# Kernel optimization log

Hardware: AMD Instinct MI355X
Metric: run time of the kernel (lower is better)

Reference implementation:

```python
import jax, jax.numpy as jnp
import numpy as np

B, H, OUT = 16384, 1024, 128
W_SCALE = 0.03  # ~1/sqrt(H) so attention logits / softmax stay well-conditioned


def setup_inputs() -> dict:
    key = jax.random.key(0)
    ks = jax.random.split(key, 12)
    return {
        "f1": jax.random.normal(ks[0], (B, H), jnp.float32),
        "f2": jax.random.normal(ks[1], (B, H), jnp.float32),
        "f3": jax.random.normal(ks[2], (B, H), jnp.float32),
        "f4": jax.random.normal(ks[3], (B, H), jnp.float32),
        "Wq": jax.random.normal(ks[4], (H, H), jnp.float32) * W_SCALE,
        "bq": jax.random.normal(ks[5], (H,), jnp.float32) * W_SCALE,
        "Wk": jax.random.normal(ks[6], (H, H), jnp.float32) * W_SCALE,
        "bk": jax.random.normal(ks[7], (H,), jnp.float32) * W_SCALE,
        "Wv": jax.random.normal(ks[8], (H, H), jnp.float32) * W_SCALE,
        "bv": jax.random.normal(ks[9], (H,), jnp.float32) * W_SCALE,
        "Wfc": jax.random.normal(ks[10], (H, OUT), jnp.float32) * W_SCALE,
        "bfc": jax.random.normal(ks[11], (OUT,), jnp.float32) * W_SCALE,
    }


def reference(f1, f2, f3, f4, Wq, bq, Wk, bk, Wv, bv, Wfc, bfc):
    # Stack the 4 backbone features: z [B, 4, H]
    z = jnp.stack([f1, f2, f3, f4], axis=1)
    q = z @ Wq + bq            # [B, 4, H]
    k = z @ Wk + bk            # [B, 4, H]
    v = z @ Wv + bv            # [B, 4, H]
    # Tiny 4x4 self-attention over the 4 model-feature tokens
    score = jax.nn.softmax(jnp.einsum('bth,bsh->bts', q, k), axis=-1)  # [B,4,4]
    att = jnp.einsum('bts,bsh->bth', score, v)                          # [B,4,H]
    x = jnp.sum(att, axis=1)                                            # [B,H]
    out = jax.nn.softmax(x @ Wfc + bfc, axis=-1)                        # [B,OUT]
    return (x, out)
```

## Files before the change

### kernel.cpp

```cpp
#include <hip/hip_runtime.h>
#include <hip/hip_bf16.h>
#include <stdint.h>

#define B_SZ 16384
#define H_SZ 1024
#define OUT_SZ 128

typedef __attribute__((ext_vector_type(4))) float f32x4;
typedef __attribute__((ext_vector_type(8))) _Float16 h16x8;
typedef unsigned short u16;
typedef unsigned int u32;

__device__ __forceinline__ u16 f2h(float f) {
  union { _Float16 h; u16 u; } v; v.h = (_Float16)f; return v.u;
}
__device__ __forceinline__ float h2f(u16 u) {
  union { u16 u; _Float16 h; } v; v.u = u; return (float)v.h;
}
__device__ __forceinline__ u32 pk2(float a, float b) {
  return (u32)f2h(a) | ((u32)f2h(b) << 16);
}

__device__ __forceinline__ void gl_lds16(const void* g, void* l) {
  __builtin_amdgcn_global_load_lds(
      (const __attribute__((address_space(1))) u32*)g,
      (__attribute__((address_space(3))) u32*)l, 16, 0, 0);
}

template<int MODE>
__global__ __launch_bounds__(256, 4) void gemm_nt(
    const u16* __restrict__ Aptr, const u16* __restrict__ Bptr,
    int N, int K,
    float* __restrict__ ep_f, u16* __restrict__ ep_b,
    const float* __restrict__ ep_v,
    const float* zf0, const float* zf1, const float* zf2, const float* zf3)
{
  constexpr int BM = 128, BN = 128, BK = 32;
  __shared__ __align__(16) u16 sA[2][BM * BK];
  __shared__ __align__(16) u16 sB[2][BN * BK];
  const int tid  = threadIdx.x;
  const int wave = tid >> 6;
  const int lane = tid & 63;
  const int qd   = lane >> 4;
  const int c16  = lane & 15;
  const int bm0  = blockIdx.x * BM;
  const int bn0  = blockIdx.y * BN;
  const int wm   = (wave >> 1) * 64;
  const int wn   = (wave & 1) * 64;
  const size_t FBS = (size_t)B_SZ * H_SZ;

  auto stage = [&](int buf, int k0) {
#pragma unroll
    for (int i = 0; i < 2; ++i) {
      int slot = tid + i * 256;
      int r = slot >> 2, pp = slot & 3;
      int cc = pp ^ ((r >> 1) & 3);
      {
        int gm = bm0 + r;
        const u16* gp;
        if (MODE == 1)
          gp = Aptr + (size_t)(gm & 3) * FBS + (size_t)(gm >> 2) * H_SZ + (k0 + cc * 8);
        else
          gp = Aptr + (size_t)gm * K + (k0 + cc * 8);
        gl_lds16(gp, &sA[buf][(size_t)(slot & ~63) * 8]);
      }
      {
        int gn = bn0 + r;
        const u16* gp = Bptr + (size_t)gn * K + (k0 + cc * 8);
        gl_lds16(gp, &sB[buf][(size_t)(slot & ~63) * 8]);
      }
    }
  };

  f32x4 acc[4][4];
#pragma unroll
  for (int i = 0; i < 4; ++i)
#pragma unroll
    for (int j = 0; j < 4; ++j)
      acc[i][j] = (f32x4){0.f, 0.f, 0.f, 0.f};

  stage(0, 0);
  __syncthreads();
  int cur = 0;
  for (int k0 = 0; k0 < K; k0 += BK) {
    if (k0 + BK < K) stage(cur ^ 1, k0 + BK);
    h16x8 af[4], bfr[4];
#pragma unroll
    for (int im = 0; im < 4; ++im) {
      int m = wm + im * 16 + c16;
      int slot = m * 4 + (qd ^ ((m >> 1) & 3));
      af[im] = *(const h16x8*)&sA[cur][slot * 8];
    }
#pragma unroll
    for (int in = 0; in < 4; ++in) {
      int n = wn + in * 16 + c16;
      int slot = n * 4 + (qd ^ ((n >> 1) & 3));
      bfr[in] = *(const h16x8*)&sB[cur][slot * 8];
    }
#pragma unroll
    for (int im = 0; im < 4; ++im)
#pragma unroll
      for (int in = 0; in < 4; ++in)
        acc[im][in] = __builtin_amdgcn_mfma_f32_16x16x32_f16(af[im], bfr[in], acc[im][in], 0, 0, 0);
    __syncthreads();
    cur ^= 1;
  }

  if constexpr (MODE == 0) {
#pragma unroll
    for (int im = 0; im < 4; ++im)
#pragma unroll
      for (int in = 0; in < 4; ++in) {
        int n = bn0 + wn + in * 16 + c16;
#pragma unroll
        for (int r = 0; r < 4; ++r) {
          int m = bm0 + wm + im * 16 + qd * 4 + r;
          ep_b[(size_t)m * N + n] = f2h(acc[im][in][r]);
        }
      }
  } else if constexpr (MODE == 1) {
    const float* zf[4] = {zf0, zf1, zf2, zf3};
    const int yg = (int)blockIdx.y * 2 + (wn >> 6);
#pragma unroll
    for (int im = 0; im < 4; ++im) {
      int mrow = bm0 + wm + im * 16 + qd * 4;
      size_t b = (size_t)(mrow >> 2);
      float p[4][4];
#pragma unroll
      for (int r = 0; r < 4; ++r)
#pragma unroll
        for (int s = 0; s < 4; ++s) p[r][s] = 0.f;
#pragma unroll
      for (int in = 0; in < 4; ++in) {
        int n = bn0 + wn + in * 16 + c16;
        float akv = ep_v[n];
        float rv[4];
#pragma unroll
        for (int r = 0; r < 4; ++r) rv[r] = acc[im][in][r] + akv;
#pragma unroll
        for (int s = 0; s < 4; ++s) {
          float zv = zf[s][b * H_SZ + n];
#pragma unroll
          for (int r = 0; r < 4; ++r) p[r][s] += rv[r] * zv;
        }
      }
#pragma unroll
      for (int r = 0; r < 4; ++r)
#pragma unroll
        for (int s = 0; s < 4; ++s) {
          float v = p[r][s];
          v += __shfl_xor(v, 1);
          v += __shfl_xor(v, 2);
          v += __shfl_xor(v, 4);
          v += __shfl_xor(v, 8);
          if (c16 == 0) ep_f[(b * 16 + (size_t)(r * 4 + s)) * 16 + yg] = v;
        }
    }
  } else if constexpr (MODE == 2) {
#pragma unroll
    for (int im = 0; im < 4; ++im)
#pragma unroll
      for (int in = 0; in < 4; ++in) {
        int n = bn0 + wn + in * 16 + c16;
        float bvv = 4.0f * ep_v[n];
#pragma unroll
        for (int r = 0; r < 4; ++r) {
          int m = bm0 + wm + im * 16 + qd * 4 + r;
          float v = acc[im][in][r] + bvv;
          ep_f[(size_t)m * H_SZ + n] = v;
          ep_b[(size_t)m * H_SZ + n] = f2h(v);
        }
      }
  } else {
#pragma unroll
    for (int im = 0; im < 4; ++im)
#pragma unroll
      for (int in = 0; in < 4; ++in) {
        int n = bn0 + wn + in * 16 + c16;
        float bc = ep_v[n];
#pragma unroll
        for (int r = 0; r < 4; ++r) {
          int m = bm0 + wm + im * 16 + qd * 4 + r;
          ep_f[(size_t)m * N + n] = acc[im][in][r] + bc;
        }
      }
  }
}

__global__ __launch_bounds__(256) void prep_weights(
    const float* __restrict__ Wq, const float* __restrict__ Wk,
    const float* __restrict__ Wv, const float* __restrict__ Wfc,
    const float* __restrict__ bq,
    u16* __restrict__ Wq16, u16* __restrict__ Wk16,
    u16* __restrict__ WvT, u16* __restrict__ WfcT,
    float* __restrict__ ak)
{
  __shared__ float t[32][33];
  int blk = blockIdx.x, tid = threadIdx.x;
  if (blk < 2048) {
    const float* src = (blk < 1024) ? Wq : Wk;
    u16* dst = (blk < 1024) ? Wq16 : Wk16;
    size_t i0 = (size_t)(blk & 1023) * 1024 + tid * 4;
    float4 v = *(const float4*)(src + i0);
    *(uint2*)(dst + i0) = make_uint2(pk2(v.x, v.y), pk2(v.z, v.w));
  } else if (blk < 3200) {
    int lx = tid & 31, ly = tid >> 5;
    if (blk < 3072) {
      int ti = blk - 2048;
      int tx = ti & 31, ty = ti >> 5;
#pragma unroll
      for (int k = 0; k < 4; ++k)
        t[ly + 8 * k][lx] = Wv[(size_t)(ty * 32 + ly + 8 * k) * 1024 + tx * 32 + lx];
      __syncthreads();
#pragma unroll
      for (int k = 0; k < 4; ++k)
        WvT[(size_t)(tx * 32 + ly + 8 * k) * 1024 + ty * 32 + lx] = f2h(t[lx][ly + 8 * k]);
    } else {
      int ti = blk - 3072;
      int tx = ti & 3, ty = ti >> 2;
#pragma unroll
      for (int k = 0; k < 4; ++k)
        t[ly + 8 * k][lx] = Wfc[(size_t)(ty * 32 + ly + 8 * k) * 128 + tx * 32 + lx];
      __syncthreads();
#pragma unroll
      for (int k = 0; k < 4; ++k)
        WfcT[(size_t)(tx * 32 + ly + 8 * k) * 1024 + ty * 32 + lx] = f2h(t[lx][ly + 8 * k]);
    }
  } else {
    int wave = tid >> 6, lane = tid & 63;
    int row = (blk - 3200) * 4 + wave;
    float s = 0.f;
    for (int i = lane; i < 1024; i += 64)
      s += Wk[(size_t)row * 1024 + i] * bq[i];
#pragma unroll
    for (int m = 1; m < 64; m <<= 1) s += __shfl_xor(s, m);
    if (lane == 0) ak[row] = s;
  }
}

__global__ __launch_bounds__(256) void convert4(
    const float* __restrict__ f1, const float* __restrict__ f2,
    const float* __restrict__ f3, const float* __restrict__ f4,
    u16* __restrict__ Zh)
{
  int a = blockIdx.x >> 13;
  const float* f = (a == 0) ? f1 : (a == 1) ? f2 : (a == 2) ? f3 : f4;
  size_t off = (size_t)(blockIdx.x & 8191) * 2048 + threadIdx.x * 8;
  float4 v0 = *(const float4*)(f + off);
  float4 v1 = *(const float4*)(f + off + 4);
  *(uint4*)(Zh + (size_t)a * B_SZ * H_SZ + off) =
      make_uint4(pk2(v0.x, v0.y), pk2(v0.z, v0.w), pk2(v1.x, v1.y), pk2(v1.z, v1.w));
}

__global__ __launch_bounds__(256) void softmax_g(
    const float* __restrict__ pl, const u16* __restrict__ Zh,
    u16* __restrict__ G)
{
  const size_t FBS = (size_t)B_SZ * H_SZ;
  int wave = threadIdx.x >> 6, lane = threadIdx.x & 63;
  size_t b = (size_t)blockIdx.x * 4 + wave;
  float4 pv = *(const float4*)(pl + b * 256 + (size_t)lane * 4);
  float part = pv.x + pv.y + pv.z + pv.w;
  part += __shfl_xor(part, 1);
  part += __shfl_xor(part, 2);
  float l[16];
#pragma unroll
  for (int i = 0; i < 16; ++i) l[i] = __shfl(part, i * 4);
  float w0 = 0, w1 = 0, w2 = 0, w3 = 0;
#pragma unroll
  for (int t = 0; t < 4; ++t) {
    float a0 = l[t * 4], a1 = l[t * 4 + 1], a2 = l[t * 4 + 2], a3 = l[t * 4 + 3];
    float mx = fmaxf(fmaxf(a0, a1), fmaxf(a2, a3));
    float e0 = __expf(a0 - mx), e1 = __expf(a1 - mx), e2 = __expf(a2 - mx), e3 = __expf(a3 - mx);
    float inv = 1.0f / (e0 + e1 + e2 + e3);
    w0 += e0 * inv; w1 += e1 * inv; w2 += e2 * inv; w3 += e3 * inv;
  }
#pragma unroll
  for (int ch = 0; ch < 2; ++ch) {
    size_t h0 = (size_t)lane * 8 + ch * 512;
    float g[8];
#pragma unroll
    for (int j = 0; j < 8; ++j) g[j] = 0.f;
#pragma unroll
    for (int s = 0; s < 4; ++s) {
      float ws = (s == 0) ? w0 : (s == 1) ? w1 : (s == 2) ? w2 : w3;
      uint4 zz = *(const uint4*)(Zh + (size_t)s * FBS + b * H_SZ + h0);
      u32 zs[4] = {zz.x, zz.y, zz.z, zz.w};
#pragma unroll
      for (int j = 0; j < 4; ++j) {
        g[2 * j]     += ws * h2f((u16)(zs[j] & 0xffffu));
        g[2 * j + 1] += ws * h2f((u16)(zs[j] >> 16));
      }
    }
    *(uint4*)(G + b * H_SZ + h0) =
        make_uint4(pk2(g[0], g[1]), pk2(g[2], g[3]), pk2(g[4], g[5]), pk2(g[6], g[7]));
  }
}

__global__ __launch_bounds__(256) void softmax_out(
    const float* __restrict__ L2, float* __restrict__ out)
{
  int wave = threadIdx.x >> 6, lane = threadIdx.x & 63;
  size_t row = (size_t)blockIdx.x * 4 + wave;
  float2 v = *(const float2*)(L2 + row * 128 + lane * 2);
  float mx = fmaxf(v.x, v.y);
#pragma unroll
  for (int m = 1; m < 64; m <<= 1) mx = fmaxf(mx, __shfl_xor(mx, m));
  float e0 = __expf(v.x - mx), e1 = __expf(v.y - mx);
  float s = e0 + e1;
#pragma unroll
  for (int m = 1; m < 64; m <<= 1) s += __shfl_xor(s, m);
  float inv = 1.0f / s;
  *(float2*)(out + row * 128 + lane * 2) = make_float2(e0 * inv, e1 * inv);
}

extern "C" void kernel_launch(void* const* d_in, const int* in_sizes, int n_in,
                              void* d_out, int out_size, void* d_ws, size_t ws_size,
                              hipStream_t stream)
{
  const float* f1  = (const float*)d_in[0];
  const float* f2  = (const float*)d_in[1];
  const float* f3  = (const float*)d_in[2];
  const float* f4  = (const float*)d_in[3];
  const float* Wq  = (const float*)d_in[4];
  const float* bq  = (const float*)d_in[5];
  const float* Wk  = (const float*)d_in[6];
  const float* Wv  = (const float*)d_in[8];
  const float* bv  = (const float*)d_in[9];
  const float* Wfc = (const float*)d_in[10];
  const float* bfc = (const float*)d_in[11];

  float* x_out = (float*)d_out;
  float* out2  = x_out + (size_t)B_SZ * H_SZ;

  const size_t BH = (size_t)B_SZ * H_SZ;
  const size_t HH = (size_t)H_SZ * H_SZ;
  char* w = (char*)d_ws;
  u16* Zh   = (u16*)w;  w += 4 * BH * sizeof(u16);
  u16* G    = (u16*)w;  w += BH * sizeof(u16);
  u16* Xh   = (u16*)w;  w += BH * sizeof(u16);
  u16* Wq16 = (u16*)w;  w += HH * 2;
  u16* Wk16 = (u16*)w;  w += HH * 2;
  u16* AT   = (u16*)w;  w += HH * 2;
  u16* WvT  = (u16*)w;  w += HH * 2;
  u16* WfcT = (u16*)w;  w += (size_t)OUT_SZ * H_SZ * 2;
  float* ak  = (float*)w;  w += H_SZ * sizeof(float);
  float* fcl = (float*)w;  w += (size_t)B_SZ * OUT_SZ * sizeof(float);
  float* pl  = (float*)Xh;

  prep_weights<<<3456, 256, 0, stream>>>(Wq, Wk, Wv, Wfc, bq,
      Wq16, Wk16, WvT, WfcT, ak);
  convert4<<<32768, 256, 0, stream>>>(f1, f2, f3, f4, Zh);
  gemm_nt<0><<<dim3(8, 8), 256, 0, stream>>>(
      Wk16, Wq16, 1024, 1024, nullptr, AT, nullptr,
      nullptr, nullptr, nullptr, nullptr);
  gemm_nt<1><<<dim3(512, 8), 256, 0, stream>>>(
      Zh, AT, 1024, 1024, pl, nullptr, ak, f1, f2, f3, f4);
  softmax_g<<<4096, 256, 0, stream>>>(pl, Zh, G);
  gemm_nt<2><<<dim3(128, 8), 256, 0, stream>>>(
      G, WvT, 1024, 1024, x_out, Xh, bv,
      nullptr, nullptr, nullptr, nullptr);
  gemm_nt<3><<<dim3(128, 1), 256, 0, stream>>>(
      Xh, WfcT, 128, 1024, fcl, nullptr, bfc,
      nullptr, nullptr, nullptr, nullptr);
  softmax_out<<<4096, 256, 0, stream>>>(fcl, out2);
}
```

Baseline: 695.6 us.

## Add 256x256 tile GEMM kernel for the score and value GEMMs

Introduces a 512-thread GEMM kernel with 256x256 output tiles, a K-step of 64 and an XOR-swizzled LDS layout. It is used for the large Z·Aᵀ score-partial GEMM and the G·Wvᵀ GEMM, while the older 128x128 kernel is kept for the small GEMMs. Larger tiles raise operand reuse and cut global and L2 traffic per MFMA. The cost is 128KB of double-buffered LDS per block, so only one block fits per CU, and the value GEMM launches just 256 blocks, which lowers occupancy and latency hiding.

```diff
diff --git a/kernel.cpp b/kernel.cpp
--- a/kernel.cpp
+++ b/kernel.cpp
@@ -25,6 +25,142 @@
   __builtin_amdgcn_global_load_lds(
       (const __attribute__((address_space(1))) u32*)g,
       (__attribute__((address_space(3))) u32*)l, 16, 0, 0);
+}
+
+template<int MODE>
+__global__ __launch_bounds__(512, 2) void gemm_nt256(
+    const u16* __restrict__ Aptr, const u16* __restrict__ Bptr,
+    int K,
+    float* __restrict__ ep_f, u16* __restrict__ ep_b,
+    const float* __restrict__ ep_v,
+    const float* zf0, const float* zf1, const float* zf2, const float* zf3)
+{
+  constexpr int BM = 256, BN = 256, BK = 64;
+  __shared__ __align__(16) u16 sA[2][BM * BK];
+  __shared__ __align__(16) u16 sB[2][BN * BK];
+  const int tid  = threadIdx.x;
+  const int wave = tid >> 6;
+  const int lane = tid & 63;
+  const int qd   = lane >> 4;
+  const int c16  = lane & 15;
+  const int bm0  = blockIdx.x * BM;
+  const int bn0  = blockIdx.y * BN;
+  const int wm   = (wave >> 2) * 128;
+  const int wn   = (wave & 3) * 64;
+  const size_t FBS = (size_t)B_SZ * H_SZ;
+
+  auto stage = [&](int buf, int k0) {
+#pragma unroll
+    for (int i = 0; i < 4; ++i) {
+      int slot = tid + i * 512;
+      int r = slot >> 3, c = slot & 7;
+      int cc = c ^ (r & 7);
+      {
+        int gm = bm0 + r;
+        const u16* gp;
+        if (MODE == 1)
+          gp = Aptr + (size_t)(gm & 3) * FBS + (size_t)(gm >> 2) * H_SZ + (k0 + cc * 8);
+        else
+          gp = Aptr + (size_t)gm * K + (k0 + cc * 8);
+        gl_lds16(gp, &sA[buf][(size_t)(slot & ~63) * 8]);
+      }
+      {
+        int gn = bn0 + r;
+        const u16* gp = Bptr + (size_t)gn * K + (k0 + cc * 8);
+        gl_lds16(gp, &sB[buf][(size_t)(slot & ~63) * 8]);
+      }
+    }
+  };
+
+  f32x4 acc[8][4];
+#pragma unroll
+  for (int i = 0; i < 8; ++i)
+#pragma unroll
+    for (int j = 0; j < 4; ++j)
+      acc[i][j] = (f32x4){0.f, 0.f, 0.f, 0.f};
+
+  stage(0, 0);
+  __syncthreads();
+  int cur = 0;
+  for (int k0 = 0; k0 < K; k0 += BK) {
+    if (k0 + BK < K) stage(cur ^ 1, k0 + BK);
+#pragma unroll
+    for (int ks = 0; ks < 2; ++ks) {
+      h16x8 af[8], bfr[4];
+#pragma unroll
+      for (int im = 0; im < 8; ++im) {
+        int m = wm + im * 16 + c16;
+        af[im] = *(const h16x8*)&sA[cur][m * 64 + (((ks * 4 + qd) ^ (m & 7)) * 8)];
+      }
+#pragma unroll
+      for (int in = 0; in < 4; ++in) {
+        int n = wn + in * 16 + c16;
+        bfr[in] = *(const h16x8*)&sB[cur][n * 64 + (((ks * 4 + qd) ^ (n & 7)) * 8)];
+      }
+#pragma unroll
+      for (int im = 0; im < 8; ++im)
+#pragma unroll
+        for (int in = 0; in < 4; ++in)
+          acc[im][in] = __builtin_amdgcn_mfma_f32_16x16x32_f16(af[im], bfr[in], acc[im][in], 0, 0, 0);
+    }
+    __syncthreads();
+    cur ^= 1;
+  }
+
+  if constexpr (MODE == 1) {
+    const float* zf[4] = {zf0, zf1, zf2, zf3};
+    const int yg = (int)blockIdx.y * 4 + (wave & 3);
+#pragma unroll
+    for (int im = 0; im < 8; ++im) {
+      int mrow = bm0 + wm + im * 16 + qd * 4;
+      size_t b = (size_t)(mrow >> 2);
+      float p[4][4];
+#pragma unroll
+      for (int r = 0; r < 4; ++r)
+#pragma unroll
+        for (int s = 0; s < 4; ++s) p[r][s] = 0.f;
+#pragma unroll
+      for (int in = 0; in < 4; ++in) {
+        int n = bn0 + wn + in * 16 + c16;
+        float akv = ep_v[n];
+        float rv[4];
+#pragma unroll
+        for (int r = 0; r < 4; ++r) rv[r] = acc[im][in][r] + akv;
+#pragma unroll
+        for (int s = 0; s < 4; ++s) {
+          float zv = zf[s][b * H_SZ + n];
+#pragma unroll
+          for (int r = 0; r < 4; ++r) p[r][s] += rv[r] * zv;
+        }
+      }
+#pragma unroll
+      for (int r = 0; r < 4; ++r)
+#pragma unroll
+        for (int s = 0; s < 4; ++s) {
+          float v = p[r][s];
+          v += __shfl_xor(v, 1);
+          v += __shfl_xor(v, 2);
+          v += __shfl_xor(v, 4);
+          v += __shfl_xor(v, 8);
+          if (c16 == 0) ep_f[(b * 16 + (size_t)(r * 4 + s)) * 16 + yg] = v;
+        }
+    }
+  } else {
+#pragma unroll
+    for (int im = 0; im < 8; ++im)
+#pragma unroll
+      for (int in = 0; in < 4; ++in) {
+        int n = bn0 + wn + in * 16 + c16;
+        float bvv = 4.0f * ep_v[n];
+#pragma unroll
+        for (int r = 0; r < 4; ++r) {
+          int m = bm0 + wm + im * 16 + qd * 4 + r;
+          float v = acc[im][in][r] + bvv;
+          ep_f[(size_t)m * H_SZ + n] = v;
+          ep_b[(size_t)m * H_SZ + n] = f2h(v);
+        }
+      }
+  }
 }
 
 template<int MODE>
@@ -32,8 +168,7 @@
     const u16* __restrict__ Aptr, const u16* __restrict__ Bptr,
     int N, int K,
     float* __restrict__ ep_f, u16* __restrict__ ep_b,
-    const float* __restrict__ ep_v,
-    const float* zf0, const float* zf1, const float* zf2, const float* zf3)
+    const float* __restrict__ ep_v)
 {
   constexpr int BM = 128, BN = 128, BK = 32;
   __shared__ __align__(16) u16 sA[2][BM * BK];
@@ -47,7 +182,6 @@
   const int bn0  = blockIdx.y * BN;
   const int wm   = (wave >> 1) * 64;
   const int wn   = (wave & 1) * 64;
-  const size_t FBS = (size_t)B_SZ * H_SZ;
 
   auto stage = [&](int buf, int k0) {
 #pragma unroll
@@ -57,11 +191,7 @@
       int cc = pp ^ ((r >> 1) & 3);
       {
         int gm = bm0 + r;
-        const u16* gp;
-        if (MODE == 1)
-          gp = Aptr + (size_t)(gm & 3) * FBS + (size_t)(gm >> 2) * H_SZ + (k0 + cc * 8);
-        else
-          gp = Aptr + (size_t)gm * K + (k0 + cc * 8);
+        const u16* gp = Aptr + (size_t)gm * K + (k0 + cc * 8);
         gl_lds16(gp, &sA[buf][(size_t)(slot & ~63) * 8]);
       }
       {
@@ -116,59 +246,6 @@
         for (int r = 0; r < 4; ++r) {
           int m = bm0 + wm + im * 16 + qd * 4 + r;
           ep_b[(size_t)m * N + n] = f2h(acc[im][in][r]);
-        }
-      }
-  } else if constexpr (MODE == 1) {
-    const float* zf[4] = {zf0, zf1, zf2, zf3};
-    const int yg = (int)blockIdx.y * 2 + (wn >> 6);
-#pragma unroll
-    for (int im = 0; im < 4; ++im) {
-      int mrow = bm0 + wm + im * 16 + qd * 4;
-      size_t b = (size_t)(mrow >> 2);
-      float p[4][4];
-#pragma unroll
-      for (int r = 0; r < 4; ++r)
-#pragma unroll
-        for (int s = 0; s < 4; ++s) p[r][s] = 0.f;
-#pragma unroll
-      for (int in = 0; in < 4; ++in) {
-        int n = bn0 + wn + in * 16 + c16;
-        float akv = ep_v[n];
-        float rv[4];
-#pragma unroll
-        for (int r = 0; r < 4; ++r) rv[r] = acc[im][in][r] + akv;
-#pragma unroll
-        for (int s = 0; s < 4; ++s) {
-          float zv = zf[s][b * H_SZ + n];
-#pragma unroll
-          for (int r = 0; r < 4; ++r) p[r][s] += rv[r] * zv;
-        }
-      }
-#pragma unroll
-      for (int r = 0; r < 4; ++r)
-#pragma unroll
-        for (int s = 0; s < 4; ++s) {
-          float v = p[r][s];
-          v += __shfl_xor(v, 1);
-          v += __shfl_xor(v, 2);
-          v += __shfl_xor(v, 4);
-          v += __shfl_xor(v, 8);
-          if (c16 == 0) ep_f[(b * 16 + (size_t)(r * 4 + s)) * 16 + yg] = v;
-        }
-    }
-  } else if constexpr (MODE == 2) {
-#pragma unroll
-    for (int im = 0; im < 4; ++im)
-#pragma unroll
-      for (int in = 0; in < 4; ++in) {
-        int n = bn0 + wn + in * 16 + c16;
-        float bvv = 4.0f * ep_v[n];
-#pragma unroll
-        for (int r = 0; r < 4; ++r) {
-          int m = bm0 + wm + im * 16 + qd * 4 + r;
-          float v = acc[im][in][r] + bvv;
-          ep_f[(size_t)m * H_SZ + n] = v;
-          ep_b[(size_t)m * H_SZ + n] = f2h(v);
         }
       }
   } else {
@@ -352,16 +429,14 @@
       Wq16, Wk16, WvT, WfcT, ak);
   convert4<<<32768, 256, 0, stream>>>(f1, f2, f3, f4, Zh);
   gemm_nt<0><<<dim3(8, 8), 256, 0, stream>>>(
-      Wk16, Wq16, 1024, 1024, nullptr, AT, nullptr,
-      nullptr, nullptr, nullptr, nullptr);
-  gemm_nt<1><<<dim3(512, 8), 256, 0, stream>>>(
-      Zh, AT, 1024, 1024, pl, nullptr, ak, f1, f2, f3, f4);
+      Wk16, Wq16, 1024, 1024, nullptr, AT, nullptr);
+  gemm_nt256<1><<<dim3(256, 4), 512, 0, stream>>>(
+      Zh, AT, 1024, pl, nullptr, ak, f1, f2, f3, f4);
   softmax_g<<<4096, 256, 0, stream>>>(pl, Zh, G);
-  gemm_nt<2><<<dim3(128, 8), 256, 0, stream>>>(
-      G, WvT, 1024, 1024, x_out, Xh, bv,
+  gemm_nt256<2><<<dim3(64, 4), 512, 0, stream>>>(
+      G, WvT, 1024, x_out, Xh, bv,
       nullptr, nullptr, nullptr, nullptr);
   gemm_nt<3><<<dim3(128, 1), 256, 0, stream>>>(
-      Xh, WfcT, 128, 1024, fcl, nullptr, bfc,
-      nullptr, nullptr, nullptr, nullptr);
+      Xh, WfcT, 128, 1024, fcl, nullptr, bfc);
   softmax_out<<<4096, 256, 0, stream>>>(fcl, out2);
 }
```

Result: no change. 686.0 us (-1.4%).
